# Kernel optimization log

Hardware: AMD Instinct MI355X
Metric: run time of the kernel (lower is better)

Reference implementation:

```python
import jax, jax.numpy as jnp
import numpy as np

PAD = 0
CONST_NO = 10000   # ids > CONST_NO are variables
N_PRED = 50
B, S, G = 8, 64, 8
F, R, BMAX = 200000, 200, 3
K_F, K_R = 64, 32  # max fact / rule children per state


def _is_var(x):
    return x > CONST_NO


def setup_inputs() -> dict:
    key = jax.random.key(0)
    ks = jax.random.split(key, 12)
    # facts: (pred, arg0, arg1), preds in [1, N_PRED], args are constants
    fp = jax.random.randint(ks[0], (F, 1), 1, N_PRED + 1, dtype=jnp.int32)
    fa = jax.random.randint(ks[1], (F, 2), 1, CONST_NO + 1, dtype=jnp.int32)
    facts = jnp.concatenate([fp, fa], axis=1)
    fact_scores = jax.random.uniform(ks[2], (F,), jnp.float32, 0.1, 1.0)
    # rule heads: p(V1, V2) with V1 = CONST_NO+1, V2 = CONST_NO+2
    hp = jax.random.randint(ks[3], (R, 1), 1, N_PRED + 1, dtype=jnp.int32)
    heads = jnp.concatenate([hp,
                             jnp.full((R, 1), CONST_NO + 1, jnp.int32),
                             jnp.full((R, 1), CONST_NO + 2, jnp.int32)], axis=1)
    # rule bodies: args are head vars or fresh constants
    bp = jax.random.randint(ks[4], (R, BMAX, 1), 1, N_PRED + 1, dtype=jnp.int32)
    choice = jax.random.randint(ks[5], (R, BMAX, 2), 0, 3, dtype=jnp.int32)
    consts = jax.random.randint(ks[6], (R, BMAX, 2), 1, CONST_NO + 1, dtype=jnp.int32)
    bargs = jnp.where(choice == 0, CONST_NO + 1,
                      jnp.where(choice == 1, CONST_NO + 2, consts)).astype(jnp.int32)
    bodies = jnp.concatenate([bp, bargs], axis=2)
    rule_lens = jax.random.randint(ks[7], (R,), 1, BMAX + 1, dtype=jnp.int32)
    rule_scores = jax.random.uniform(ks[8], (R,), jnp.float32, 0.1, 1.0)
    # proof goals [B,S,G,3]: args mix of constants and query vars CONST_NO+3/+4
    gp = jax.random.randint(ks[9], (B, S, G, 1), 1, N_PRED + 1, dtype=jnp.int32)
    vch = jax.random.randint(ks[10], (B, S, G, 2), 0, 4, dtype=jnp.int32)
    gc = jax.random.randint(ks[11], (B, S, G, 2), 1, CONST_NO + 1, dtype=jnp.int32)
    gargs = jnp.where(vch == 0, CONST_NO + 3,
                      jnp.where(vch == 1, CONST_NO + 4, gc)).astype(jnp.int32)
    goals = jnp.concatenate([gp, gargs], axis=3)
    # variable number of live goals per state (tail padded)
    pos = jnp.arange(G)
    keep = jax.random.randint(jax.random.fold_in(key, 99), (B, S, 1), 1, G + 1, dtype=jnp.int32)
    goals = jnp.where(pos[None, None, :, None] < keep[..., None], goals, PAD)
    state_scores = jax.random.uniform(jax.random.fold_in(key, 7), (B, S), jnp.float32, 0.1, 1.0)
    return dict(proof_goals=goals, state_scores=state_scores, facts=facts,
                fact_scores=fact_scores, heads=heads, bodies=bodies,
                rule_lens=rule_lens, rule_scores=rule_scores)


def reference(proof_goals, state_scores, facts, fact_scores, heads, bodies, rule_lens, rule_scores):
    # ---- 1. SELECT: query = goal slot 0, remaining goals mask slot 0 ----
    q = proof_goals[:, :, 0]                         # [B,S,3]
    active = q[..., 0] != PAD                        # [B,S]
    remaining = proof_goals.at[:, :, 0, :].set(PAD)  # [B,S,G,3]
    qp, qa0, qa1 = q[..., 0], q[..., 1], q[..., 2]

    # ---- 2. RESOLVE FACTS: unify query against fact table ----
    m = ((qp[..., None] == facts[:, 0])
         & (_is_var(qa0)[..., None] | (qa0[..., None] == facts[:, 1]))
         & (_is_var(qa1)[..., None] | (qa1[..., None] == facts[:, 2]))
         & active[..., None])                        # [B,S,F]
    fvals, fidx = jax.lax.top_k(m.astype(jnp.int32), K_F)
    fact_success = fvals > 0                         # [B,S,K_f]
    mf = facts[fidx]                                 # [B,S,K_f,3]
    # substitute query variables with matched fact constants in remaining goals
    v0 = qa0[:, :, None, None, None]
    v1 = qa1[:, :, None, None, None]
    b0 = mf[..., 1][..., None, None]
    b1 = mf[..., 2][..., None, None]
    rem = remaining[:, :, None]                      # [B,S,1,G,3]
    fg = jnp.where(_is_var(v0) & (rem == v0), b0, rem)
    fg = jnp.where(_is_var(v1) & (fg == v1), b1, fg)  # [B,S,K_f,G,3]
    fsc = jnp.where(fact_success, state_scores[:, :, None] * fact_scores[fidx], 0.0)

    # ---- 3. RESOLVE RULES: unify query against rule heads, append bodies ----
    mr = ((qp[..., None] == heads[:, 0])
          & (_is_var(heads[:, 1]) | _is_var(qa0)[..., None] | (qa0[..., None] == heads[:, 1]))
          & (_is_var(heads[:, 2]) | _is_var(qa1)[..., None] | (qa1[..., None] == heads[:, 2]))
          & active[..., None])                       # [B,S,R]
    rvals, ridx = jax.lax.top_k(mr.astype(jnp.int32), K_R)
    rule_success = rvals > 0                         # [B,S,K_r]
    mh = heads[ridx]                                 # [B,S,K_r,3]
    body = bodies[ridx]                              # [B,S,K_r,BMAX,3]
    h0 = mh[..., 1][..., None, None]
    h1 = mh[..., 2][..., None, None]
    qa0b = qa0[:, :, None, None, None]
    qa1b = qa1[:, :, None, None, None]
    body = jnp.where(_is_var(h0) & (body == h0), qa0b, body)
    body = jnp.where(_is_var(h1) & (body == h1), qa1b, body)
    bmask = jnp.arange(BMAX) < rule_lens[ridx][..., None]    # [B,S,K_r,BMAX]
    body = jnp.where(bmask[..., None], body, PAD)
    rem_rest = jnp.broadcast_to(remaining[:, :, None, 1:1 + (G - BMAX)], (B, S, K_R, G - BMAX, 3))
    rg = jnp.concatenate([body, rem_rest], axis=3)   # [B,S,K_r,G,3]
    rsc = jnp.where(rule_success, state_scores[:, :, None] * rule_scores[ridx], 0.0)

    # ---- 4. PACK: flatten SxK children, compact successful ones to S states ----
    K = K_F + K_R
    all_goals = jnp.concatenate([fg, rg], axis=2).reshape(B, S * K, G, 3)
    all_succ = jnp.concatenate([fact_success, rule_success], axis=2).reshape(B, S * K)
    all_sc = jnp.concatenate([fsc, rsc], axis=2).reshape(B, S * K)
    pvals, pidx = jax.lax.top_k(all_succ.astype(jnp.int32), S)
    new_succ = pvals > 0                             # [B,S]
    new_goals = jnp.take_along_axis(all_goals, pidx[..., None, None], axis=1)
    # ---- 5. POSTPROCESS: zero out failed / padded states ----
    new_goals = jnp.where(new_succ[..., None, None], new_goals, PAD)
    new_scores = jnp.where(new_succ, jnp.take_along_axis(all_sc, pidx, axis=1), 0.0)
    return new_goals, new_scores
```

## Files before the change

kernel.cpp:

```cpp
#include <hip/hip_runtime.h>

#define PAD 0
#define CONST_NO 10000
#define Bn 8
#define Sn 64
#define Gn 8
#define Fn 200000
#define Rn 200
#define BMAXn 3
#define KF 64
#define KR 32

#define NBLK 196
#define CHB  1024

#define OFF_CNTF   0
#define OFF_PN     512
#define OFF_PFIRST 1024
#define OFF_UF     5120

__device__ __forceinline__ bool isv(int x) { return x > CONST_NO; }

__global__ __launch_bounds__(256) void probe_kernel(
    const int* __restrict__ goals, const int* __restrict__ facts,
    int* __restrict__ ws)
{
    const int t = threadIdx.x;
    const int lane = t & 63, wv = t >> 6;

    if (blockIdx.x < NBLK) {
        __shared__ int4 qlist[512];
        __shared__ int qcnt[64], qstart[64];
        const int B = blockIdx.x;

        if (t < 64) qcnt[t] = 0;
        __syncthreads();

        int myPos[2], myQp[2], myQv[2], myQm[2], mySt[2];
        #pragma unroll
        for (int k = 0; k < 2; ++k) {
            const int s = t + k * 256;
            const int* q = goals + s * (Gn * 3);
            const int qp = q[0], qa0 = q[1], qa1 = q[2];
            const bool v0 = isv(qa0), v1 = isv(qa1);
            const bool use = (qp != PAD) && !(v0 && v1);
            myQp[k] = use ? qp : -1;
            myQv[k] = (v0 ? 0 : (qa0 << 14)) | (v1 ? 0 : qa1);
            myQm[k] = (v0 ? 0 : (0x3FFF << 14)) | (v1 ? 0 : 0x3FFF);
            mySt[k] = s;
            myPos[k] = use ? atomicAdd(&qcnt[qp], 1) : -1;
        }
        __syncthreads();
        if (t < 64) {
            const int v = qcnt[t];
            int incl = v;
            #pragma unroll
            for (int off = 1; off < 64; off <<= 1) {
                int n = __shfl_up(incl, off, 64);
                if (t >= off) incl += n;
            }
            qstart[t] = incl - v;
        }
        __syncthreads();
        #pragma unroll
        for (int k = 0; k < 2; ++k)
            if (myQp[k] >= 0)
                qlist[qstart[myQp[k]] + myPos[k]] =
                    make_int4(myQv[k], myQm[k], mySt[k], 0);
        __syncthreads();

        const int f0 = B * CHB + t * 4;
        int pv[4], pk[4];
        if (f0 + 3 < Fn) {
            const int4* p4 = (const int4*)(facts + 3 * f0);
            int4 a = p4[0], b4 = p4[1], c4 = p4[2];
            pv[0] = a.x;  pk[0] = (a.y  << 14) | a.z;
            pv[1] = a.w;  pk[1] = (b4.x << 14) | b4.y;
            pv[2] = b4.z; pk[2] = (b4.w << 14) | c4.x;
            pv[3] = c4.y; pk[3] = (c4.z << 14) | c4.w;
        } else {
            #pragma unroll
            for (int u = 0; u < 4; ++u) {
                pv[u] = -1; pk[u] = 0;
                if (f0 + u < Fn) {
                    pv[u] = facts[3 * (f0 + u)];
                    pk[u] = (facts[3 * (f0 + u) + 1] << 14) | facts[3 * (f0 + u) + 2];
                }
            }
        }
        #pragma unroll
        for (int u = 0; u < 4; ++u) {
            if (pv[u] >= 0) {
                const int j0 = qstart[pv[u]], j1 = j0 + qcnt[pv[u]];
                for (int j = j0; j < j1; ++j) {
                    const int4 qq = qlist[j];
                    if (((pk[u] ^ qq.x) & qq.y) == 0) {
                        const int pos = atomicAdd(ws + OFF_CNTF + qq.z, 1);
                        if (pos < KF) ws[OFF_UF + qq.z * KF + pos] = f0 + u;
                    }
                }
            }
        }
    } else {
        __shared__ int wave_tot[4];
        const int p = blockIdx.x - NBLK + 1;

        int total = 0;
        for (int base = 0; base < Fn && total < KF; base += 1024) {
            const int f0 = base + t * 4;
            unsigned mbits = 0;
            if (f0 + 3 < Fn) {
                const int4* p4 = (const int4*)(facts + 3 * f0);
                int4 a = p4[0], b4 = p4[1], c4 = p4[2];
                if (a.x  == p) mbits |= 1u;
                if (a.w  == p) mbits |= 2u;
                if (b4.z == p) mbits |= 4u;
                if (c4.y == p) mbits |= 8u;
            } else {
                #pragma unroll
                for (int u = 0; u < 4; ++u)
                    if (f0 + u < Fn && facts[3 * (f0 + u)] == p) mbits |= (1u << u);
            }
            const int c4n = __popc(mbits);

            int v = c4n;
            #pragma unroll
            for (int off = 1; off < 64; off <<= 1) {
                int n = __shfl_up(v, off, 64);
                if (lane >= off) v += n;
            }
            if (lane == 63) wave_tot[wv] = v;
            __syncthreads();
            int excl = v - c4n;
            #pragma unroll
            for (int w = 0; w < 4; ++w) if (w < wv) excl += wave_tot[w];
            const int ctot = wave_tot[0] + wave_tot[1] + wave_tot[2] + wave_tot[3];

            int pos = total + excl;
            #pragma unroll
            for (int u = 0; u < 4; ++u) {
                if (mbits & (1u << u)) {
                    if (pos < KF) ws[OFF_PFIRST + p * 64 + pos] = f0 + u;
                    pos++;
                }
            }
            total += ctot;
            __syncthreads();
        }
        if (t == 0) ws[OFF_PN + p] = (total < KF) ? total : KF;
    }
}

__global__ __launch_bounds__(256) void finalize_kernel(
    const int* __restrict__ goals, const float* __restrict__ ss,
    const int* __restrict__ facts, const float* __restrict__ fsc,
    const int* __restrict__ heads, const int* __restrict__ bodies,
    const int* __restrict__ rlens, const float* __restrict__ rsc,
    const int* __restrict__ ws, float* __restrict__ outp)
{
    __shared__ int sfx[Sn * 64];
    __shared__ int seg[4][Sn][16];
    __shared__ int segc[4][Sn];
    __shared__ int hds[Rn * 3];
    __shared__ int pref[Sn + 1];
    __shared__ int nfs[Sn], nrs[Sn], vvf[Sn], qps[Sn];

    const int b = blockIdx.x, t = threadIdx.x;
    const int lane = t & 63, wv = t >> 6;

    for (int k = t; k < Rn * 3; k += 256) hds[k] = heads[k];
    segc[wv][lane] = 0;
    __syncthreads();

    {
        const int s = lane;
        const int* q = goals + (b * Sn + s) * (Gn * 3);
        const int qp = q[0], qa0 = q[1], qa1 = q[2];
        const bool v0 = isv(qa0), v1 = isv(qa1);
        const bool active = (qp != PAD);
        int cnt = 0;
        const int r0 = wv * 50;
        for (int r = r0; r < r0 + 50; ++r) {
            const int h0 = hds[3 * r], h1 = hds[3 * r + 1], h2 = hds[3 * r + 2];
            if (active && h0 == qp && (isv(h1) || v0 || qa0 == h1)
                                   && (isv(h2) || v1 || qa1 == h2)) {
                if (cnt < 16) seg[wv][s][cnt] = r;
                cnt++;
            }
        }
        segc[wv][s] = (cnt < 16) ? cnt : 16;
    }
    __syncthreads();

    if (t < Sn) {
        const int s = t;
        const int* q = goals + (b * Sn + s) * (Gn * 3);
        const int qp = q[0], qa0 = q[1], qa1 = q[2];
        const bool v0 = isv(qa0), v1 = isv(qa1);
        const bool active = (qp != PAD);
        const bool vv = active && v0 && v1;
        int nf = 0;
        if (vv) {
            nf = ws[OFF_PN + qp];
        } else if (active) {
            int c = ws[OFF_CNTF + b * Sn + s];
            if (c > KF) c = KF;
            for (int j = 0; j < c; ++j)
                sfx[s * 64 + j] = ws[OFF_UF + (b * Sn + s) * KF + j];
            for (int a = 1; a < c; ++a) {
                const int key = sfx[s * 64 + a];
                int m = a - 1;
                while (m >= 0 && sfx[s * 64 + m] > key) {
                    sfx[s * 64 + m + 1] = sfx[s * 64 + m];
                    m--;
                }
                sfx[s * 64 + m + 1] = key;
            }
            nf = c;
        }
        nfs[s] = nf;
        vvf[s] = vv ? 1 : 0;
        qps[s] = qp;
        int nr = segc[0][s] + segc[1][s] + segc[2][s] + segc[3][s];
        if (nr > KR) nr = KR;
        nrs[s] = nr;

        int incl = nf + nr;
        #pragma unroll
        for (int off = 1; off < 64; off <<= 1) {
            int n = __shfl_up(incl, off, 64);
            if (t >= off) incl += n;
        }
        pref[s + 1] = incl;
        if (s == 0) pref[0] = 0;
    }
    __syncthreads();
    const int total = pref[Sn];

    for (int item = t; item < Sn * Gn; item += 256) {
        const int i = item >> 3, g = item & 7;
        int trip[3] = {PAD, PAD, PAD};
        if (i < total) {
            int lo = 0, hi = Sn - 1;
            while (lo < hi) {
                const int mid = (lo + hi) >> 1;
                if (pref[mid + 1] <= i) lo = mid + 1; else hi = mid;
            }
            const int s = lo, j = i - pref[s];
            const int* q = goals + (b * Sn + s) * (Gn * 3);
            const int qa0 = q[1], qa1 = q[2];
            if (j < nfs[s]) {
                const int fi = vvf[s] ? ws[OFF_PFIRST + qps[s] * 64 + j]
                                      : sfx[s * 64 + j];
                const int f1 = facts[3 * fi + 1], f2 = facts[3 * fi + 2];
                if (g >= 1) {
                    #pragma unroll
                    for (int c = 0; c < 3; ++c) {
                        int x = q[g * 3 + c];
                        if (isv(qa0) && x == qa0) x = f1;
                        else if (isv(qa1) && x == qa1) x = f2;
                        trip[c] = x;
                    }
                }
            } else {
                int jr = j - nfs[s];
                int wz = 0;
                while (jr >= segc[wz][s]) { jr -= segc[wz][s]; wz++; }
                const int ri = seg[wz][s][jr];
                const int h1 = hds[3 * ri + 1], h2 = hds[3 * ri + 2];
                const int len = rlens[ri];
                if (g < BMAXn) {
                    if (g < len) {
                        #pragma unroll
                        for (int c = 0; c < 3; ++c) {
                            int x = bodies[(ri * BMAXn + g) * 3 + c];
                            if (isv(h1) && x == h1) x = qa0;
                            if (isv(h2) && x == h2) x = qa1;
                            trip[c] = x;
                        }
                    }
                } else {
                    trip[0] = q[(g - 2) * 3 + 0];
                    trip[1] = q[(g - 2) * 3 + 1];
                    trip[2] = q[(g - 2) * 3 + 2];
                }
            }
        }
        float* o = outp + ((b * Sn + i) * Gn + g) * 3;
        o[0] = (float)trip[0];
        o[1] = (float)trip[1];
        o[2] = (float)trip[2];
    }

    if (t < Sn) {
        const int i = t;
        float sc = 0.f;
        if (i < total) {
            int lo = 0, hi = Sn - 1;
            while (lo < hi) {
                const int mid = (lo + hi) >> 1;
                if (pref[mid + 1] <= i) lo = mid + 1; else hi = mid;
            }
            const int s = lo, j = i - pref[s];
            const float stt = ss[b * Sn + s];
            if (j < nfs[s]) {
                const int fi = vvf[s] ? ws[OFF_PFIRST + qps[s] * 64 + j]
                                      : sfx[s * 64 + j];
                sc = stt * fsc[fi];
            } else {
                int jr = j - nfs[s];
                int wz = 0;
                while (jr >= segc[wz][s]) { jr -= segc[wz][s]; wz++; }
                sc = stt * rsc[seg[wz][s][jr]];
            }
        }
        outp[Bn * Sn * Gn * 3 + b * Sn + t] = sc;
    }
}

extern "C" void kernel_launch(void* const* d_in, const int* in_sizes, int n_in,
                              void* d_out, int out_size, void* d_ws, size_t ws_size,
                              hipStream_t stream) {
    const int*   goals  = (const int*)  d_in[0];
    const float* ss     = (const float*)d_in[1];
    const int*   facts  = (const int*)  d_in[2];
    const float* fsc    = (const float*)d_in[3];
    const int*   heads  = (const int*)  d_in[4];
    const int*   bodies = (const int*)  d_in[5];
    const int*   rlens  = (const int*)  d_in[6];
    const float* rsc    = (const float*)d_in[7];
    int*   ws   = (int*)d_ws;
    float* outp = (float*)d_out;

    hipMemsetAsync(ws, 0, 512 * sizeof(int), stream);
    probe_kernel   <<<NBLK + 50, 256, 0, stream>>>(goals, facts, ws);
    finalize_kernel<<<Bn,        256, 0, stream>>>(goals, ss, facts, fsc, heads,
                                                   bodies, rlens, rsc, ws, outp);
}
```

Measured before the change: 90.51 us.

## Buffer fact matches per block in LDS and drop the workspace memset

The probe kernel now collects matching (state, fact) pairs into a shared-memory buffer per block, packing the state index into the high bits. It then writes that buffer to a per-block region of the workspace, replacing the global atomics on per-state counters. The finalize kernel prefix-sums the block counts, gathers all entries into LDS, and each state scans the whole list for its own matches. Because every block writes its own count, the hipMemsetAsync launch is no longer needed. The costs are a linear scan by each state thread over up to 1024 entries and silent truncation if a block has more than 128 matches or the total exceeds 1024.

Measured after the change: 95.98 us. +6.1%, slower.

```diff
diff --git a/kernel.cpp b/kernel.cpp
--- a/kernel.cpp
+++ b/kernel.cpp
@@ -13,11 +13,12 @@
 
 #define NBLK 196
 #define CHB  1024
-
-#define OFF_CNTF   0
-#define OFF_PN     512
-#define OFF_PFIRST 1024
-#define OFF_UF     5120
+#define BCAP 128
+
+#define OFF_BCNT   0
+#define OFF_BENT   200
+#define OFF_PN     (200 + NBLK * BCAP)
+#define OFF_PFIRST (OFF_PN + 64)
 
 __device__ __forceinline__ bool isv(int x) { return x > CONST_NO; }
 
@@ -31,12 +32,15 @@
     if (blockIdx.x < NBLK) {
         __shared__ int4 qlist[512];
         __shared__ int qcnt[64], qstart[64];
+        __shared__ int ebuf[BCAP];
+        __shared__ int ecnt;
         const int B = blockIdx.x;
 
         if (t < 64) qcnt[t] = 0;
-        __syncthreads();
-
-        int myPos[2], myQp[2], myQv[2], myQm[2], mySt[2];
+        if (t == 0) ecnt = 0;
+        __syncthreads();
+
+        int myPos[2], myQp[2], myQv[2], myQm[2];
         #pragma unroll
         for (int k = 0; k < 2; ++k) {
             const int s = t + k * 256;
@@ -47,7 +51,6 @@
             myQp[k] = use ? qp : -1;
             myQv[k] = (v0 ? 0 : (qa0 << 14)) | (v1 ? 0 : qa1);
             myQm[k] = (v0 ? 0 : (0x3FFF << 14)) | (v1 ? 0 : 0x3FFF);
-            mySt[k] = s;
             myPos[k] = use ? atomicAdd(&qcnt[qp], 1) : -1;
         }
         __syncthreads();
@@ -66,7 +69,7 @@
         for (int k = 0; k < 2; ++k)
             if (myQp[k] >= 0)
                 qlist[qstart[myQp[k]] + myPos[k]] =
-                    make_int4(myQv[k], myQm[k], mySt[k], 0);
+                    make_int4(myQv[k], myQm[k], (t + k * 256) << 18, 0);
         __syncthreads();
 
         const int f0 = B * CHB + t * 4;
@@ -95,12 +98,16 @@
                 for (int j = j0; j < j1; ++j) {
                     const int4 qq = qlist[j];
                     if (((pk[u] ^ qq.x) & qq.y) == 0) {
-                        const int pos = atomicAdd(ws + OFF_CNTF + qq.z, 1);
-                        if (pos < KF) ws[OFF_UF + qq.z * KF + pos] = f0 + u;
+                        const int pos = atomicAdd(&ecnt, 1);
+                        if (pos < BCAP) ebuf[pos] = qq.z | (f0 + u);
                     }
                 }
             }
         }
+        __syncthreads();
+        const int n = (ecnt < BCAP) ? ecnt : BCAP;
+        if (t == 0) ws[OFF_BCNT + B] = n;
+        if (t < n) ws[OFF_BENT + B * BCAP + t] = ebuf[t];
     } else {
         __shared__ int wave_tot[4];
         const int p = blockIdx.x - NBLK + 1;
@@ -159,18 +166,46 @@
     const int* __restrict__ ws, float* __restrict__ outp)
 {
     __shared__ int sfx[Sn * 64];
+    __shared__ int E[1024];
+    __shared__ int base[256];
+    __shared__ int wtot[4];
     __shared__ int seg[4][Sn][16];
     __shared__ int segc[4][Sn];
     __shared__ int hds[Rn * 3];
     __shared__ int pref[Sn + 1];
-    __shared__ int nfs[Sn], nrs[Sn], vvf[Sn], qps[Sn];
+    __shared__ int nfs[Sn], vvf[Sn], qps[Sn];
 
     const int b = blockIdx.x, t = threadIdx.x;
     const int lane = t & 63, wv = t >> 6;
 
     for (int k = t; k < Rn * 3; k += 256) hds[k] = heads[k];
     segc[wv][lane] = 0;
+
+    const int myc = (t < NBLK) ? ws[OFF_BCNT + t] : 0;
+    {
+        int incl = myc;
+        #pragma unroll
+        for (int off = 1; off < 64; off <<= 1) {
+            int n = __shfl_up(incl, off, 64);
+            if (lane >= off) incl += n;
+        }
+        if (lane == 63) wtot[wv] = incl;
+        __syncthreads();
+        int excl = incl - myc;
+        #pragma unroll
+        for (int w = 0; w < 4; ++w) if (w < wv) excl += wtot[w];
+        base[t] = excl;
+    }
     __syncthreads();
+    const int totalE0 = wtot[0] + wtot[1] + wtot[2] + wtot[3];
+    const int totalE = (totalE0 < 1024) ? totalE0 : 1024;
+
+    if (t < NBLK) {
+        for (int k = 0; k < myc; ++k) {
+            const int dst = base[t] + k;
+            if (dst < 1024) E[dst] = ws[OFF_BENT + t * BCAP + k];
+        }
+    }
 
     {
         const int s = lane;
@@ -194,7 +229,8 @@
 
     if (t < Sn) {
         const int s = t;
-        const int* q = goals + (b * Sn + s) * (Gn * 3);
+        const int gs = b * Sn + s;
+        const int* q = goals + gs * (Gn * 3);
         const int qp = q[0], qa0 = q[1], qa1 = q[2];
         const bool v0 = isv(qa0), v1 = isv(qa1);
         const bool active = (qp != PAD);
@@ -203,11 +239,12 @@
         if (vv) {
             nf = ws[OFF_PN + qp];
         } else if (active) {
-            int c = ws[OFF_CNTF + b * Sn + s];
-            if (c > KF) c = KF;
-            for (int j = 0; j < c; ++j)
-                sfx[s * 64 + j] = ws[OFF_UF + (b * Sn + s) * KF + j];
-            for (int a = 1; a < c; ++a) {
+            for (int i = 0; i < totalE; ++i) {
+                const int e = E[i];
+                if ((e >> 18) == gs && nf < KF)
+                    sfx[s * 64 + nf++] = e & 0x3FFFF;
+            }
+            for (int a = 1; a < nf; ++a) {
                 const int key = sfx[s * 64 + a];
                 int m = a - 1;
                 while (m >= 0 && sfx[s * 64 + m] > key) {
@@ -216,14 +253,12 @@
                 }
                 sfx[s * 64 + m + 1] = key;
             }
-            nf = c;
         }
         nfs[s] = nf;
         vvf[s] = vv ? 1 : 0;
         qps[s] = qp;
         int nr = segc[0][s] + segc[1][s] + segc[2][s] + segc[3][s];
         if (nr > KR) nr = KR;
-        nrs[s] = nr;
 
         int incl = nf + nr;
         #pragma unroll
@@ -332,7 +367,6 @@
     int*   ws   = (int*)d_ws;
     float* outp = (float*)d_out;
 
-    hipMemsetAsync(ws, 0, 512 * sizeof(int), stream);
     probe_kernel   <<<NBLK + 50, 256, 0, stream>>>(goals, facts, ws);
     finalize_kernel<<<Bn,        256, 0, stream>>>(goals, ss, facts, fsc, heads,
                                                    bodies, rlens, rsc, ws, outp);
```
